# Kernel optimization log

Hardware: AMD Instinct MI355X
Metric: run time of the kernel (lower is better)

Reference implementation:

```python
import jax, jax.numpy as jnp
import numpy as np


def sparsemax(z):
    # Sparsemax along last axis: Euclidean projection of z onto the simplex.
    S = z.shape[-1]
    z_sorted = jnp.flip(jnp.sort(z, axis=-1), axis=-1)          # descending
    cssv = jnp.cumsum(z_sorted, axis=-1)                         # cumulative sums
    r = jnp.arange(1, S + 1, dtype=z.dtype)                      # 1..S
    support = 1.0 + r * z_sorted > cssv                          # support mask
    k = jnp.sum(support, axis=-1, keepdims=True)                 # support size (int)
    tau = (jnp.take_along_axis(cssv, k - 1, axis=-1) - 1.0) / k.astype(z.dtype)
    return jnp.maximum(z - tau, 0.0)


def setup_inputs() -> dict:
    key = jax.random.key(0)
    k1, k2, k3 = jax.random.split(key, 3)
    B, L, S, H, E, D = 8, 1024, 1024, 16, 64, 64
    queries = jax.random.normal(k1, (B, L, H, E), dtype=jnp.float32)
    keys = jax.random.normal(k2, (B, S, H, E), dtype=jnp.float32)
    values = jax.random.normal(k3, (B, S, H, D), dtype=jnp.float32)
    return {"queries": queries, "keys": keys, "values": values}


def reference(queries, keys, values):
    E = queries.shape[-1]
    scale = 1.0 / jnp.sqrt(jnp.asarray(E, dtype=queries.dtype))
    # [B,H,L,S] attention scores
    scores = jnp.einsum('blhe,bshe->bhls', queries, keys)
    A = sparsemax(scale * scores)                                # sparsemax normalization (dropout p=0)
    attn_output = jnp.einsum('bhls,bshd->blhd', A, values)
    return attn_output
```

## Files before the change

kernel.cpp:

```cpp
#include <hip/hip_runtime.h>


typedef _Float16 f16x8 __attribute__((ext_vector_type(8)));
typedef float    f32x4 __attribute__((ext_vector_type(4)));

constexpr int kB = 8, kL = 1024, kS = 1024, kH = 16, kE = 64, kD = 64;
constexpr int LT   = 32;
constexpr int JT   = 128;
constexpr int CAP  = 144;
constexpr int KMAX = CAP / 16;

__device__ __forceinline__ float pk2(float a, float b) {
  auto h = __builtin_amdgcn_cvt_pkrtz(a, b);
  return __builtin_bit_cast(float, h);
}

__device__ __forceinline__ float unpack_z(unsigned v) {
  return __uint_as_float((v & ~1023u) | 512u);
}

__global__ __launch_bounds__(512, 4)
void sparsemax_attn(const float* __restrict__ Q, const float* __restrict__ K,
                    const float* __restrict__ V, float* __restrict__ O) {
  __shared__ float4   Ksh[JT * 8];
  __shared__ float4   Qsh[LT * 8];
  __shared__ unsigned lists[LT * CAP];
  __shared__ int      cnt_s[LT];
  __shared__ float    rmax_s[LT][4];
  __shared__ float    tau_s[LT];

  const int t = threadIdx.x, lane = t & 63, w = t >> 6;
  const int qg = w >> 2, jg = w & 3;
  const int li = lane & 15, g = lane >> 4;
  const int myrow = qg * 16 + li;

  const int id  = blockIdx.x;
  const int xcd = id & 7, kk = id >> 3;
  const int bh  = xcd * 16 + (kk >> 5);
  const int b   = bh >> 4, h = bh & 15;
  const int l0  = (kk & 31) * LT;

  const float* Kbh = K + ((size_t)b * kS * kH + h) * kE;
  const float* Vb  = V + ((size_t)b * kS * kH + h) * kD;

  if (t < LT) cnt_s[t] = 0;
  if (t >= 384 && t < 512) ((float*)rmax_s)[t - 384] = -1e30f;
  if (t < 256) {
    const int jj = t >> 3, e8 = t & 7;
    const float4* qp =
        (const float4*)(Q + (((size_t)(b * kL + l0 + jj)) * kH + h) * kE + e8 * 8);
    float4 q0 = qp[0], q1 = qp[1];
    q0.x *= .125f; q0.y *= .125f; q0.z *= .125f; q0.w *= .125f;
    q1.x *= .125f; q1.y *= .125f; q1.z *= .125f; q1.w *= .125f;
    Qsh[jj * 8 + (e8 ^ (jj & 7))] =
        make_float4(pk2(q0.x, q0.y), pk2(q0.z, q0.w), pk2(q1.x, q1.y), pk2(q1.z, q1.w));
  }

  float runl = -1e30f;
  f16x8 b0, b1;

  for (int jt = 0; jt < kS / JT; ++jt) {
    __syncthreads();
#pragma unroll
    for (int i = 0; i < 2; ++i) {
      const int idx = t + 512 * i, jj = idx >> 3, e8 = idx & 7;
      const float4* kp =
          (const float4*)(Kbh + (size_t)(jt * JT + jj) * (kH * kE) + e8 * 8);
      const float4 c0 = kp[0], c1 = kp[1];
      Ksh[jj * 8 + (e8 ^ (jj & 7))] =
          make_float4(pk2(c0.x, c0.y), pk2(c0.z, c0.w), pk2(c1.x, c1.y), pk2(c1.z, c1.w));
    }
    __syncthreads();
    if (jt == 0) {
      b0 = __builtin_bit_cast(f16x8, Qsh[myrow * 8 + ((0 + g) ^ (myrow & 7))]);
      b1 = __builtin_bit_cast(f16x8, Qsh[myrow * 8 + ((4 + g) ^ (myrow & 7))]);
    }

    f32x4 acc[2];
    acc[0] = f32x4{0.f, 0.f, 0.f, 0.f};
    acc[1] = f32x4{0.f, 0.f, 0.f, 0.f};
#pragma unroll
    for (int ct = 0; ct < 2; ++ct) {
      const int jl = jg * 32 + ct * 16 + li;
      const f16x8 a0 = __builtin_bit_cast(f16x8, Ksh[jl * 8 + ((0 + g) ^ (jl & 7))]);
      const f16x8 a1 = __builtin_bit_cast(f16x8, Ksh[jl * 8 + ((4 + g) ^ (jl & 7))]);
      acc[ct] = __builtin_amdgcn_mfma_f32_16x16x32_f16(a0, b0, acc[ct], 0, 0, 0);
      acc[ct] = __builtin_amdgcn_mfma_f32_16x16x32_f16(a1, b1, acc[ct], 0, 0, 0);
    }

    const float m01 = fmaxf(fmaxf(acc[0][0], acc[0][1]), fmaxf(acc[0][2], acc[0][3]));
    const float m23 = fmaxf(fmaxf(acc[1][0], acc[1][1]), fmaxf(acc[1][2], acc[1][3]));
    runl = fmaxf(runl, fmaxf(m01, m23));
    float mr = fmaxf(runl, __shfl_xor(runl, 16));
    mr = fmaxf(mr, __shfl_xor(mr, 32));
    if (lane < 16) rmax_s[myrow][jg] = mr;
    float rm = fmaxf(fmaxf(rmax_s[myrow][0], rmax_s[myrow][1]),
                     fmaxf(rmax_s[myrow][2], rmax_s[myrow][3]));
    const float thr = fmaxf(rm, mr) - 1.0f;
    const int jbase = jt * JT + jg * 32 + g * 4;
#pragma unroll
    for (int ct = 0; ct < 2; ++ct)
#pragma unroll
      for (int r = 0; r < 4; ++r) {
        const float z = acc[ct][r];
        if (z > thr) {
          const int pos = atomicAdd(&cnt_s[myrow], 1);
          if (pos < CAP)
            lists[myrow * CAP + pos] =
                (__float_as_uint(z) & ~1023u) | (unsigned)(jbase + ct * 16 + r);
        }
      }
  }
  __syncthreads();

  const int q0 = w * 4;
  {
    const int row = q0 + g;
    const int n   = cnt_s[row];
    const int nc  = min(n, CAP);
    float zr[KMAX];
#pragma unroll
    for (int k = 0; k < KMAX; ++k) {
      const int i = li + 16 * k;
      zr[k] = (i < nc) ? unpack_z(lists[row * CAP + i]) : -1e30f;
    }
    const float M =
        fmaxf(fmaxf(rmax_s[row][0], rmax_s[row][1]), fmaxf(rmax_s[row][2], rmax_s[row][3]));
    float t0 = M - 1.0f;
    for (int it = 0; it < 14; ++it) {
      float s = 0.f, c = 0.f;
#pragma unroll
      for (int k = 0; k < KMAX; ++k) {
        const float d = zr[k] - t0;
        if (d > 0.f) { s += d; c += 1.f; }
      }
      s += __shfl_xor(s, 1); c += __shfl_xor(c, 1);
      s += __shfl_xor(s, 2); c += __shfl_xor(c, 2);
      s += __shfl_xor(s, 4); c += __shfl_xor(c, 4);
      s += __shfl_xor(s, 8); c += __shfl_xor(c, 8);
      const float delta = (s - 1.0f) / fmaxf(c, 1.f);
      t0 += fmaxf(delta, 0.f);
      if (__all(delta <= 1e-6f)) break;
    }
    if (li == 0) tau_s[row] = t0;
  }

#pragma unroll 1
  for (int r4 = 0; r4 < 4; ++r4) {
    const int row = q0 + r4;
    const int n   = cnt_s[row];
    const size_t obase = (((size_t)(b * kL + l0 + row)) * kH + h) * kD;
    if (n <= CAP) {
      const float tau = tau_s[row];
      const int nc = n;
      f32x4 o4 = {0.f, 0.f, 0.f, 0.f};
      for (int i = g; i < nc; i += 8) {
        const int   i2 = i + 4;
        const bool  ok2 = (i2 < nc);
        const unsigned e1 = lists[row * CAP + i];
        const unsigned e2 = lists[row * CAP + (ok2 ? i2 : i)];
        const float  p1 = fmaxf(unpack_z(e1) - tau, 0.f);
        const float  p2 = ok2 ? fmaxf(unpack_z(e2) - tau, 0.f) : 0.f;
        const float4 v1 =
            ((const float4*)(Vb + (size_t)(e1 & 1023u) * (kH * kD)))[li];
        const float4 v2 =
            ((const float4*)(Vb + (size_t)(e2 & 1023u) * (kH * kD)))[li];
        o4.x = fmaf(p1, v1.x, fmaf(p2, v2.x, o4.x));
        o4.y = fmaf(p1, v1.y, fmaf(p2, v2.y, o4.y));
        o4.z = fmaf(p1, v1.z, fmaf(p2, v2.z, o4.z));
        o4.w = fmaf(p1, v1.w, fmaf(p2, v2.w, o4.w));
      }
      o4.x += __shfl_xor(o4.x, 16); o4.y += __shfl_xor(o4.y, 16);
      o4.z += __shfl_xor(o4.z, 16); o4.w += __shfl_xor(o4.w, 16);
      o4.x += __shfl_xor(o4.x, 32); o4.y += __shfl_xor(o4.y, 32);
      o4.z += __shfl_xor(o4.z, 32); o4.w += __shfl_xor(o4.w, 32);
      if (lane < 16)
        ((float4*)(O + obase))[li] = make_float4(o4.x, o4.y, o4.z, o4.w);
    } else {
      float scr2[16];
      for (int cc = 0; cc < 16; ++cc) {
        const int j = lane + 64 * cc;
        const float* kr = Kbh + (size_t)j * (kH * kE);
        float zz = 0.f;
        for (int e8 = 0; e8 < 8; ++e8) {
          const f16x8 qh = __builtin_bit_cast(f16x8, Qsh[row * 8 + (e8 ^ (row & 7))]);
          const float4* kp = (const float4*)(kr + e8 * 8);
          const float4 c0 = kp[0], c1 = kp[1];
          zz += (float)qh[0] * c0.x + (float)qh[1] * c0.y + (float)qh[2] * c0.z +
                (float)qh[3] * c0.w + (float)qh[4] * c1.x + (float)qh[5] * c1.y +
                (float)qh[6] * c1.z + (float)qh[7] * c1.w;
        }
        scr2[cc] = zz;
      }
      const float M2 =
          fmaxf(fmaxf(rmax_s[row][0], rmax_s[row][1]), fmaxf(rmax_s[row][2], rmax_s[row][3]));
      float t0 = M2 - 1.0f;
      for (int it = 0; it < 48; ++it) {
        float s = 0.f, c = 0.f;
        for (int cc = 0; cc < 16; ++cc) {
          const float d = scr2[cc] - t0;
          if (d > 0.f) { s += d; c += 1.f; }
        }
        for (int off = 32; off; off >>= 1) { s += __shfl_xor(s, off); c += __shfl_xor(c, off); }
        const float delta = (s - 1.0f) / fmaxf(c, 1.f);
        if (delta <= 1e-7f) break;
        t0 += delta;
      }
      float oacc = 0.f;
      for (int cc = 0; cc < 16; ++cc)
        for (int src = 0; src < 64; ++src) {
          const float z = __shfl(scr2[cc], src);
          const float p = z - t0;
          if (p > 0.f)
            oacc = fmaf(p, Vb[(size_t)(src + 64 * cc) * (kH * kD) + lane], oacc);
        }
      O[obase + lane] = oacc;
    }
  }
}

extern "C" void kernel_launch(void* const* d_in, const int* in_sizes, int n_in,
                              void* d_out, int out_size, void* d_ws, size_t ws_size,
                              hipStream_t stream) {
  (void)in_sizes; (void)n_in; (void)out_size; (void)d_ws; (void)ws_size;
  const float* Q = (const float*)d_in[0];
  const float* K = (const float*)d_in[1];
  const float* V = (const float*)d_in[2];
  float* O = (float*)d_out;
  sparsemax_attn<<<dim3(kB * kH * (kL / LT)), dim3(512), 0, stream>>>(Q, K, V, O);
}
```

Before: 406.7 us.

## Double-buffer K tiles in shared memory with register prefetch, shrink candidate list cap

K tiles are now staged through two shared-memory buffers. The next tile is loaded into registers two iterations ahead, so global-load latency overlaps the MFMA and candidate-filtering work and one barrier per iteration is dropped. The candidate list capacity is also cut from 144 to 96 to offset the extra shared memory and cut per-row register use in the tau solve. The risk is more rows overflowing the list and taking the slow fallback path, plus higher register pressure from the prefetched float4s.

```diff
diff --git a/kernel.cpp b/kernel.cpp
--- a/kernel.cpp
+++ b/kernel.cpp
@@ -7,7 +7,8 @@
 constexpr int kB = 8, kL = 1024, kS = 1024, kH = 16, kE = 64, kD = 64;
 constexpr int LT   = 32;
 constexpr int JT   = 128;
-constexpr int CAP  = 144;
+constexpr int NT   = kS / JT;
+constexpr int CAP  = 96;
 constexpr int KMAX = CAP / 16;
 
 __device__ __forceinline__ float pk2(float a, float b) {
@@ -22,7 +23,7 @@
 __global__ __launch_bounds__(512, 4)
 void sparsemax_attn(const float* __restrict__ Q, const float* __restrict__ K,
                     const float* __restrict__ V, float* __restrict__ O) {
-  __shared__ float4   Ksh[JT * 8];
+  __shared__ float4   Ksh[2][JT * 8];
   __shared__ float4   Qsh[LT * 8];
   __shared__ unsigned lists[LT * CAP];
   __shared__ int      cnt_s[LT];
@@ -42,6 +43,14 @@
 
   const float* Kbh = K + ((size_t)b * kS * kH + h) * kE;
   const float* Vb  = V + ((size_t)b * kS * kH + h) * kD;
+
+  const int jj0 = t >> 3, e8_0 = t & 7;
+  const int jj1 = (t + 512) >> 3, e8_1 = t & 7;
+  const float4* kp0 = (const float4*)(Kbh + (size_t)jj0 * (kH * kE) + e8_0 * 8);
+  const float4* kp1 = (const float4*)(Kbh + (size_t)jj1 * (kH * kE) + e8_1 * 8);
+  const int slot0 = jj0 * 8 + (e8_0 ^ (jj0 & 7));
+  const int slot1 = jj1 * 8 + (e8_1 ^ (jj1 & 7));
+  constexpr size_t tileStride = (size_t)JT * kH * kE / 4;
 
   if (t < LT) cnt_s[t] = 0;
   if (t >= 384 && t < 512) ((float*)rmax_s)[t - 384] = -1e30f;
@@ -56,20 +65,21 @@
         make_float4(pk2(q0.x, q0.y), pk2(q0.z, q0.w), pk2(q1.x, q1.y), pk2(q1.z, q1.w));
   }
 
+  float4 pf0a, pf0b, pf1a, pf1b;
+
+  pf0a = kp0[0]; pf0b = kp0[1]; pf1a = kp1[0]; pf1b = kp1[1];
+  Ksh[0][slot0] = make_float4(pk2(pf0a.x, pf0a.y), pk2(pf0a.z, pf0a.w),
+                              pk2(pf0b.x, pf0b.y), pk2(pf0b.z, pf0b.w));
+  Ksh[0][slot1] = make_float4(pk2(pf1a.x, pf1a.y), pk2(pf1a.z, pf1a.w),
+                              pk2(pf1b.x, pf1b.y), pk2(pf1b.z, pf1b.w));
+  pf0a = kp0[tileStride]; pf0b = kp0[tileStride + 1];
+  pf1a = kp1[tileStride]; pf1b = kp1[tileStride + 1];
+
   float runl = -1e30f;
   f16x8 b0, b1;
 
-  for (int jt = 0; jt < kS / JT; ++jt) {
-    __syncthreads();
-#pragma unroll
-    for (int i = 0; i < 2; ++i) {
-      const int idx = t + 512 * i, jj = idx >> 3, e8 = idx & 7;
-      const float4* kp =
-          (const float4*)(Kbh + (size_t)(jt * JT + jj) * (kH * kE) + e8 * 8);
-      const float4 c0 = kp[0], c1 = kp[1];
-      Ksh[jj * 8 + (e8 ^ (jj & 7))] =
-          make_float4(pk2(c0.x, c0.y), pk2(c0.z, c0.w), pk2(c1.x, c1.y), pk2(c1.z, c1.w));
-    }
+  for (int jt = 0; jt < NT; ++jt) {
+    const int cur = jt & 1;
     __syncthreads();
     if (jt == 0) {
       b0 = __builtin_bit_cast(f16x8, Qsh[myrow * 8 + ((0 + g) ^ (myrow & 7))]);
@@ -82,8 +92,8 @@
 #pragma unroll
     for (int ct = 0; ct < 2; ++ct) {
       const int jl = jg * 32 + ct * 16 + li;
-      const f16x8 a0 = __builtin_bit_cast(f16x8, Ksh[jl * 8 + ((0 + g) ^ (jl & 7))]);
-      const f16x8 a1 = __builtin_bit_cast(f16x8, Ksh[jl * 8 + ((4 + g) ^ (jl & 7))]);
+      const f16x8 a0 = __builtin_bit_cast(f16x8, Ksh[cur][jl * 8 + ((0 + g) ^ (jl & 7))]);
+      const f16x8 a1 = __builtin_bit_cast(f16x8, Ksh[cur][jl * 8 + ((4 + g) ^ (jl & 7))]);
       acc[ct] = __builtin_amdgcn_mfma_f32_16x16x32_f16(a0, b0, acc[ct], 0, 0, 0);
       acc[ct] = __builtin_amdgcn_mfma_f32_16x16x32_f16(a1, b1, acc[ct], 0, 0, 0);
     }
@@ -110,6 +120,18 @@
                 (__float_as_uint(z) & ~1023u) | (unsigned)(jbase + ct * 16 + r);
         }
       }
+
+    if (jt < NT - 1) {
+      Ksh[cur ^ 1][slot0] = make_float4(pk2(pf0a.x, pf0a.y), pk2(pf0a.z, pf0a.w),
+                                        pk2(pf0b.x, pf0b.y), pk2(pf0b.z, pf0b.w));
+      Ksh[cur ^ 1][slot1] = make_float4(pk2(pf1a.x, pf1a.y), pk2(pf1a.z, pf1a.w),
+                                        pk2(pf1b.x, pf1b.y), pk2(pf1b.z, pf1b.w));
+      if (jt < NT - 2) {
+        const size_t off = (size_t)(jt + 2) * tileStride;
+        pf0a = kp0[off]; pf0b = kp0[off + 1];
+        pf1a = kp1[off]; pf1b = kp1[off + 1];
+      }
+    }
   }
   __syncthreads();
 
```

Measured after the change: 514.2 us. 26.4% more time.
